# Optimization experiments

Hardware: AMD Instinct MI355X
Metric: run time of the kernel (lower is better)

## Reference

```python
import jax, jax.numpy as jnp
import numpy as np

N = 100000      # nodes
IN_DIM = 128    # input feature dim
HID = 64        # hidden_dim / out_dim per head
HEADS = 4
E_RAND = 1600000  # random edges; self-loops appended -> E = E_RAND + N
SCALES = 3


def setup_inputs() -> dict:
    key = jax.random.key(0)
    ks = jax.random.split(key, 12)
    h = jax.random.normal(ks[0], (N, IN_DIM), dtype=jnp.float32)
    src = jax.random.randint(ks[1], (E_RAND,), 0, N)
    dst = jax.random.randint(ks[2], (E_RAND,), 0, N)
    loop = jnp.arange(N)
    src = jnp.concatenate([src, loop])  # self-loops ensure every dst has a mailbox
    dst = jnp.concatenate([dst, loop])
    frac_cover_mat = jax.random.randint(ks[3], (N, SCALES), 0, N)
    # learned params (bias=False everywhere); xavier-ish scaling
    layer1_fc = jax.random.normal(ks[4], (HEADS, HID, IN_DIM), jnp.float32) / np.sqrt(IN_DIM)
    layer1_attn = jax.random.normal(ks[5], (HEADS, 2 * HID), jnp.float32) * 0.1
    layer2_fc = jax.random.normal(ks[6], (HID, HID * HEADS), jnp.float32) / np.sqrt(HID * HEADS)
    layer2_attn = jax.random.normal(ks[7], (2 * HID,), jnp.float32) * 0.1
    frac_w = jax.random.normal(ks[8], (SCALES, HID, IN_DIM), jnp.float32) / np.sqrt(IN_DIM)
    frac_final_w = jax.random.normal(ks[9], (HID, SCALES * HID), jnp.float32) / np.sqrt(SCALES * HID)
    fc2_w = jax.random.normal(ks[10], (HID, 2 * HID), jnp.float32) / np.sqrt(2 * HID)
    return {"h": h, "src": src, "dst": dst, "frac_cover_mat": frac_cover_mat,
            "layer1_fc": layer1_fc, "layer1_attn": layer1_attn,
            "layer2_fc": layer2_fc, "layer2_attn": layer2_attn,
            "frac_w": frac_w, "frac_final_w": frac_final_w, "fc2_w": fc2_w}


def _gat_layer(z, src, dst, attn_w, n):
    # attn(cat([z_src, z_dst])) == z_src @ a_src + z_dst @ a_dst  (bias-free Linear)
    d = z.shape[1]
    e = jax.nn.leaky_relu(z[src] @ attn_w[:d] + z[dst] @ attn_w[d:])  # [E]
    # segment softmax over incoming edges of each dst node
    m = jax.ops.segment_max(e, dst, num_segments=n)
    ex = jnp.exp(e - m[dst])
    denom = jax.ops.segment_sum(ex, dst, num_segments=n)
    alpha = ex / denom[dst]                                   # [E]
    return jax.ops.segment_sum(alpha[:, None] * z[src], dst, num_segments=n)  # [N, d]


def reference(h, src, dst, frac_cover_mat,
              layer1_fc, layer1_attn, layer2_fc, layer2_attn,
              frac_w, frac_final_w, fc2_w):
    n = h.shape[0]
    # layer1: multi-head GAT, merge='cat'
    heads = []
    for i in range(layer1_fc.shape[0]):
        z = h @ layer1_fc[i].T                                # [N, HID]
        heads.append(_gat_layer(z, src, dst, layer1_attn[i], n))
    h_nei = jax.nn.elu(jnp.concatenate(heads, axis=1))        # [N, HID*HEADS]
    # layer2: single-head GAT
    z2 = h_nei @ layer2_fc.T                                  # [N, HID]
    h_nei = _gat_layer(z2, src, dst, layer2_attn, n)          # [N, HID]
    # fractal layer (dropout = identity in eval)
    h_all = [h[frac_cover_mat[:, s]] @ frac_w[s].T for s in range(frac_w.shape[0])]
    h_frac = jnp.concatenate(h_all, axis=1) @ frac_final_w.T  # [N, HID]
    # fc2 on cat([h_nei, h_frac]); dropout identity
    h_global = jnp.concatenate([h_nei, h_frac], axis=1) @ fc2_w.T  # [N, HID]
    # AvgPooling over single graph -> [1, HID]
    return jnp.mean(h_global, axis=0, keepdims=True)
```

## Files before the change

kernel.cpp:

```cpp
#include <hip/hip_runtime.h>
#include <math.h>


#define CAP 128

typedef unsigned int  uint_t;
typedef unsigned short ushort_t;
typedef __attribute__((ext_vector_type(8))) short short8;
typedef __attribute__((ext_vector_type(4))) float floatx4;
typedef __attribute__((ext_vector_type(2))) float floatx2;

__device__ __forceinline__ float wred_sum(float v){
#pragma unroll
  for (int o = 1; o < 64; o <<= 1) v += __shfl_xor(v, o, 64);
  return v;
}
__device__ __forceinline__ float lrelu(float x){ return x >= 0.f ? x : 0.01f*x; }
__device__ __forceinline__ ushort_t f2b(float f){
  uint_t u = __float_as_uint(f);
  u = (u + 0x7FFFu + ((u >> 16) & 1u)) >> 16;
  return (ushort_t)u;
}
__device__ __forceinline__ float b2f_lo(uint_t w){ return __uint_as_float(w << 16); }
__device__ __forceinline__ float b2f_hi(uint_t w){ return __uint_as_float(w & 0xFFFF0000u); }

__global__ void k_wpack(const float* __restrict__ W1, const float* __restrict__ W2,
                        const float* __restrict__ a1, const float* __restrict__ a2,
                        ushort_t* __restrict__ w1bp, float* __restrict__ v2){
  __shared__ float v[8][128];
  const int bx = blockIdx.x, t = threadIdx.x;
  if (bx < 128){
    int idx = bx*256 + t;
    int j = idx & 7, lane = (idx >> 3) & 63, ks = (idx >> 9) & 3, tt = idx >> 11;
    int n = tt*16 + (lane & 15), k = ks*32 + (lane >> 4)*8 + j;
    w1bp[idx] = f2b(W1[n*128 + k]);
  } else if (bx == 128){
    for (int o = t; o < 1024; o += 256){
      int col = o >> 7, k = o & 127, hh = col & 3, off = (col >> 2)*64;
      float s = 0.f;
      for (int n = 0; n < 64; n++) s += a1[hh*128 + off + n] * W1[(hh*64 + n)*128 + k];
      v[col][k] = s;
    }
    __syncthreads();
    for (int idx = t; idx < 2048; idx += 256){
      int j = idx & 7, lane = (idx >> 3) & 63, ks = idx >> 9;
      int col = lane & 15, k = ks*32 + (lane >> 4)*8 + j;
      w1bp[32768 + idx] = (col < 8) ? f2b(v[col][k]) : (ushort_t)0;
    }
  } else {
    float s0 = 0.f, s1 = 0.f;
    for (int j = 0; j < 64; j++){
      float wjk = W2[j*256 + t];
      s0 += wjk * a2[j];
      s1 += wjk * a2[64 + j];
    }
    v2[t] = s0; v2[256 + t] = s1;
  }
}

__global__ __launch_bounds__(512) void k_gemm1m(const float* __restrict__ h,
    const ushort_t* __restrict__ w1bp,
    uint_t* __restrict__ z8, float* __restrict__ s1s, float* __restrict__ s1d, int N)
{
  __shared__ __align__(16) ushort_t ldsB[34816];
  const int tid = threadIdx.x;
  {
    const uint4* src = (const uint4*)w1bp;
    uint4* dst = (uint4*)ldsB;
    for (int i = tid; i < 4352; i += 512) dst[i] = src[i];
  }
  __syncthreads();
  const int wave = tid >> 6, lane = tid & 63;
  const int quad = lane >> 4, l16 = lane & 15;
  const int row0 = blockIdx.x*128 + wave*16;
  if (row0 >= N) return;
  const int ar = (row0 + l16 < N) ? (row0 + l16) : (N - 1);
  floatx4 c[17];
#pragma unroll
  for (int t = 0; t < 17; t++) c[t] = (floatx4){0.f,0.f,0.f,0.f};
#pragma unroll
  for (int ks = 0; ks < 4; ks++){
    const float* ap = &h[(size_t)ar*128 + ks*32 + quad*8];
    float4 v0 = *(const float4*)ap;
    float4 v1 = *(const float4*)(ap + 4);
    float vv[8] = {v0.x,v0.y,v0.z,v0.w,v1.x,v1.y,v1.z,v1.w};
    short8 ahi, alo;
#pragma unroll
    for (int j = 0; j < 8; j++){
      ushort_t hb = f2b(vv[j]);
      float hf = __uint_as_float((uint_t)hb << 16);
      ahi[j] = (short)hb;
      alo[j] = (short)f2b(vv[j] - hf);
    }
#pragma unroll
    for (int t = 0; t < 17; t++){
      short8 b = *(const short8*)&ldsB[(size_t)((t*4 + ks)*64 + lane)*8];
      c[t] = __builtin_amdgcn_mfma_f32_16x16x32_bf16(ahi, b, c[t], 0, 0, 0);
    }
    {
      short8 b = *(const short8*)&ldsB[(size_t)((16*4 + ks)*64 + lane)*8];
      c[16] = __builtin_amdgcn_mfma_f32_16x16x32_bf16(alo, b, c[16], 0, 0, 0);
    }
  }
#pragma unroll
  for (int i = 0; i < 4; i++){
    const int r = row0 + quad*4 + i;
    if (r >= N) continue;
#pragma unroll
    for (int m = 0; m < 4; m++){
      int u = 0;
      u = __builtin_amdgcn_cvt_pk_fp8_f32(c[0*4+m][i], c[1*4+m][i], u, false);
      u = __builtin_amdgcn_cvt_pk_fp8_f32(c[2*4+m][i], c[3*4+m][i], u, true);
      z8[(size_t)r*64 + m*16 + l16] = (uint_t)u;
    }
    const float sv = c[16][i];
    if (l16 < 4) s1s[r*4 + l16] = sv;
    else if (l16 < 8) s1d[r*4 + (l16 - 4)] = sv;
  }
}

__global__ void k_hist(const int* __restrict__ d, int* __restrict__ deg, int E){
  int i = blockIdx.x*256 + threadIdx.x;
  if (i < E) atomicAdd(&deg[d[i]], 1);
}
__global__ __launch_bounds__(256) void k_scan1(const int* __restrict__ deg, int* __restrict__ part){
  __shared__ int tmp[256];
  int t = threadIdx.x;
  tmp[t] = deg[blockIdx.x*256 + t];
  __syncthreads();
  for (int off = 128; off > 0; off >>= 1){
    if (t < off) tmp[t] += tmp[t+off];
    __syncthreads();
  }
  if (t == 0) part[blockIdx.x] = tmp[0];
}
__global__ __launch_bounds__(512) void k_scan2(int* __restrict__ part, int B){
  __shared__ int tmp[512];
  int t = threadIdx.x;
  int v = (t < B) ? part[t] : 0;
  tmp[t] = v; __syncthreads();
  for (int off = 1; off < 512; off <<= 1){
    int x = (t >= off) ? tmp[t-off] : 0;
    __syncthreads();
    tmp[t] += x;
    __syncthreads();
  }
  if (t < B) part[t] = tmp[t] - v;
}
__global__ __launch_bounds__(256) void k_scan3(const int* __restrict__ deg, const int* __restrict__ part,
    int* __restrict__ rowptr, int* __restrict__ cursor){
  __shared__ int tmp[256];
  int t = threadIdx.x, i = blockIdx.x*256 + t;
  int v = deg[i];
  tmp[t] = v; __syncthreads();
  for (int off = 1; off < 256; off <<= 1){
    int x = (t >= off) ? tmp[t-off] : 0;
    __syncthreads();
    tmp[t] += x;
    __syncthreads();
  }
  int excl = tmp[t] - v + part[blockIdx.x];
  rowptr[i] = excl; cursor[i] = excl;
}
__global__ void k_scatter(const int* __restrict__ s, const int* __restrict__ d,
    int* __restrict__ cursor, int* __restrict__ csr, int E){
  int i = blockIdx.x*256 + threadIdx.x;
  if (i < E){
    int p = atomicAdd(&cursor[d[i]], 1);
    csr[p] = s[i];
  }
}

__global__ __launch_bounds__(256) void k_gat1(
    const uint_t* __restrict__ z8, const float* __restrict__ s1src, const float* __restrict__ s1dst,
    const int* __restrict__ rowptr, const int* __restrict__ csr, const float* __restrict__ v2,
    uint_t* __restrict__ hneib, float* __restrict__ s2s, float* __restrict__ s2d, int N)
{
  __shared__ int   sbuf[4][CAP];
  __shared__ __align__(16) float4 ebuf[4][CAP];
  __shared__ float v2s[512];
  const int tid = threadIdx.x;
  v2s[tid] = v2[tid];
  v2s[tid + 256] = v2[tid + 256];
  __syncthreads();
  const int wave = tid >> 6, lane = tid & 63;
  const int dst = blockIdx.x*4 + wave;
  if (dst >= N) return;
  const int beg = rowptr[dst];
  const int deg = rowptr[dst+1] - beg;
  const float4 sd = *(const float4*)&s1dst[dst*4];
  float t0=0.f,t1=0.f,t2=0.f,t3=0.f;
  for (int j = lane; j < deg; j += 64){
    int s = csr[beg+j];
    float4 sv = *(const float4*)&s1src[s*4];
    float4 a;
    a.x = __expf(lrelu(sv.x+sd.x)); a.y = __expf(lrelu(sv.y+sd.y));
    a.z = __expf(lrelu(sv.z+sd.z)); a.w = __expf(lrelu(sv.w+sd.w));
    if (j < CAP){ sbuf[wave][j] = s; ebuf[wave][j] = a; }
    t0 += a.x; t1 += a.y; t2 += a.z; t3 += a.w;
  }
  const float inv[4] = {1.f/wred_sum(t0), 1.f/wred_sum(t1), 1.f/wred_sum(t2), 1.f/wred_sum(t3)};
  const int eh = lane >> 5, li = lane & 31;
  float acc[2][4] = {};
  int jj = 0;
  if (deg <= CAP){
    for (; jj + 2 <= deg; jj += 2){
      const int j = jj + eh;
      int s = sbuf[wave][j]; float4 al = ebuf[wave][j];
      uint2 u = *((const uint2*)(z8 + (size_t)s*64) + li);
      floatx2 p0 = __builtin_amdgcn_cvt_pk_f32_fp8(u.x, false);
      floatx2 p1 = __builtin_amdgcn_cvt_pk_f32_fp8(u.x, true);
      floatx2 p2 = __builtin_amdgcn_cvt_pk_f32_fp8(u.y, false);
      floatx2 p3 = __builtin_amdgcn_cvt_pk_f32_fp8(u.y, true);
      acc[0][0] += al.x * p0.x;
      acc[0][1] += al.y * p0.y;
      acc[0][2] += al.z * p1.x;
      acc[0][3] += al.w * p1.y;
      acc[1][0] += al.x * p2.x;
      acc[1][1] += al.y * p2.y;
      acc[1][2] += al.z * p3.x;
      acc[1][3] += al.w * p3.y;
    }
    if (jj < deg && eh == 0){
      int s = sbuf[wave][jj]; float4 al = ebuf[wave][jj];
      uint2 u = *((const uint2*)(z8 + (size_t)s*64) + li);
      floatx2 p0 = __builtin_amdgcn_cvt_pk_f32_fp8(u.x, false);
      floatx2 p1 = __builtin_amdgcn_cvt_pk_f32_fp8(u.x, true);
      floatx2 p2 = __builtin_amdgcn_cvt_pk_f32_fp8(u.y, false);
      floatx2 p3 = __builtin_amdgcn_cvt_pk_f32_fp8(u.y, true);
      acc[0][0] += al.x * p0.x;
      acc[0][1] += al.y * p0.y;
      acc[0][2] += al.z * p1.x;
      acc[0][3] += al.w * p1.y;
      acc[1][0] += al.x * p2.x;
      acc[1][1] += al.y * p2.y;
      acc[1][2] += al.z * p3.x;
      acc[1][3] += al.w * p3.y;
    }
  } else {
    for (; jj < deg; jj += 2){
      const int j = jj + eh;
      const bool v = j < deg;
      const int jc = v ? j : jj;
      int s; float4 al;
      if (jc < CAP){ s = sbuf[wave][jc]; al = ebuf[wave][jc]; }
      else {
        s = csr[beg+jc];
        float4 sv = *(const float4*)&s1src[s*4];
        al.x = __expf(lrelu(sv.x+sd.x)); al.y = __expf(lrelu(sv.y+sd.y));
        al.z = __expf(lrelu(sv.z+sd.z)); al.w = __expf(lrelu(sv.w+sd.w));
      }
      if (!v){ al.x=0.f; al.y=0.f; al.z=0.f; al.w=0.f; }
      uint2 u = *((const uint2*)(z8 + (size_t)s*64) + li);
      floatx2 p0 = __builtin_amdgcn_cvt_pk_f32_fp8(u.x, false);
      floatx2 p1 = __builtin_amdgcn_cvt_pk_f32_fp8(u.x, true);
      floatx2 p2 = __builtin_amdgcn_cvt_pk_f32_fp8(u.y, false);
      floatx2 p3 = __builtin_amdgcn_cvt_pk_f32_fp8(u.y, true);
      acc[0][0] += al.x * p0.x;
      acc[0][1] += al.y * p0.y;
      acc[0][2] += al.z * p1.x;
      acc[0][3] += al.w * p1.y;
      acc[1][0] += al.x * p2.x;
      acc[1][1] += al.y * p2.y;
      acc[1][2] += al.z * p3.x;
      acc[1][3] += al.w * p3.y;
    }
  }
#pragma unroll
  for (int k = 0; k < 2; k++)
#pragma unroll
    for (int hh = 0; hh < 4; hh++) acc[k][hh] += __shfl_xor(acc[k][hh], 32, 64);
  const float* vv = &v2s[eh*256];
  float p = 0.f;
#pragma unroll
  for (int hh = 0; hh < 4; hh++){
    float e0 = acc[0][hh]*inv[hh]; e0 = e0 > 0.f ? e0 : expm1f(e0);
    float e1 = acc[1][hh]*inv[hh]; e1 = e1 > 0.f ? e1 : expm1f(e1);
    p += e0 * vv[hh*64 + 2*li] + e1 * vv[hh*64 + 2*li + 1];
    if (eh == 0)
      hneib[(size_t)dst*128 + hh*32 + li] = (uint_t)f2b(e0) | ((uint_t)f2b(e1) << 16);
  }
#pragma unroll
  for (int o = 1; o < 32; o <<= 1) p += __shfl_xor(p, o, 64);
  if (lane == 0)  s2s[dst] = p;
  if (lane == 32) s2d[dst] = p;
}

__global__ __launch_bounds__(256) void k_aw2(
    const float* __restrict__ s2s, const float* __restrict__ s2d,
    const int* __restrict__ rowptr, const int* __restrict__ csr,
    float* __restrict__ wsrc, int N)
{
  __shared__ int   sbuf[4][CAP];
  __shared__ float ebuf[4][CAP];
  const int wave = threadIdx.x >> 6, lane = threadIdx.x & 63;
  const int dst = blockIdx.x*4 + wave;
  if (dst >= N) return;
  const int beg = rowptr[dst], deg = rowptr[dst+1] - beg;
  const float sd = s2d[dst];
  float ts = 0.f;
  for (int j = lane; j < deg; j += 64){
    int s = csr[beg+j];
    float a = __expf(lrelu(s2s[s] + sd));
    if (j < CAP){ sbuf[wave][j] = s; ebuf[wave][j] = a; }
    ts += a;
  }
  const float inv = 1.f/wred_sum(ts);
  for (int j = lane; j < deg; j += 64){
    int s; float a;
    if (j < CAP){ s = sbuf[wave][j]; a = ebuf[wave][j]; }
    else { s = csr[beg+j]; a = __expf(lrelu(s2s[s] + sd)); }
    atomicAdd(&wsrc[s], a * inv);
  }
}

__global__ __launch_bounds__(256) void k_hsum(const uint_t* __restrict__ hneib,
    const float* __restrict__ wsrc, float* __restrict__ acc256, int N)
{
  __shared__ float pr[512];
  const int t = threadIdx.x;
  const int h2 = t >> 7, p = t & 127;
  float a0 = 0.f, a1 = 0.f;
  const int step = gridDim.x * 2;
  for (int n = blockIdx.x*2 + h2; n < N; n += step){
    float wn = wsrc[n];
    uint_t u = hneib[(size_t)n*128 + p];
    a0 += wn * b2f_lo(u);
    a1 += wn * b2f_hi(u);
  }
  pr[h2*256 + 2*p]     = a0;
  pr[h2*256 + 2*p + 1] = a1;
  __syncthreads();
  float v = pr[t] + pr[256 + t];
  int pp = t >> 1;
  int d = (pp >> 5)*64 + 2*(pp & 31) + (t & 1);
  atomicAdd(&acc256[d], v);
}

__global__ __launch_bounds__(256) void k_frac(const float* __restrict__ h,
    const int* __restrict__ fcm, float* __restrict__ accFrac, int N)
{
  __shared__ float red[8][384];
  const int tid = threadIdx.x;
  const int wave = tid >> 6, lane = tid & 63;
  const int g = lane >> 5, li = lane & 31;
  const int stream0 = blockIdx.x*8 + wave*2 + g;
  const int step = gridDim.x * 8;
  float4 a0 = {0,0,0,0}, a1 = {0,0,0,0}, a2 = {0,0,0,0};
  for (int n = stream0; n < N; n += step){
    int i0 = fcm[n*3], i1 = fcm[n*3+1], i2 = fcm[n*3+2];
    float4 v0 = *(const float4*)&h[(size_t)i0*128 + li*4];
    float4 v1 = *(const float4*)&h[(size_t)i1*128 + li*4];
    float4 v2 = *(const float4*)&h[(size_t)i2*128 + li*4];
    a0.x += v0.x; a0.y += v0.y; a0.z += v0.z; a0.w += v0.w;
    a1.x += v1.x; a1.y += v1.y; a1.z += v1.z; a1.w += v1.w;
    a2.x += v2.x; a2.y += v2.y; a2.z += v2.z; a2.w += v2.w;
  }
  const int w8 = wave*2 + g;
  *(float4*)&red[w8][0*128 + li*4] = a0;
  *(float4*)&red[w8][1*128 + li*4] = a1;
  *(float4*)&red[w8][2*128 + li*4] = a2;
  __syncthreads();
  for (int i = tid; i < 384; i += 256){
    float v = 0.f;
#pragma unroll
    for (int w = 0; w < 8; w++) v += red[w][i];
    atomicAdd(&accFrac[i], v);
  }
}

__global__ __launch_bounds__(256) void k_finalize(const float* __restrict__ acc256,
    const float* __restrict__ accFrac, const float* __restrict__ W2,
    const float* __restrict__ frw, const float* __restrict__ frf,
    const float* __restrict__ fc2, float* __restrict__ out, float invN)
{
  __shared__ float mh[256], nei[64], g[384], mm[192], hfrac[64];
  int t = threadIdx.x;
  mh[t] = acc256[t] * invN;
  for (int i = t; i < 384; i += 256) g[i] = accFrac[i] * invN;
  __syncthreads();
  if (t < 64){
    float s = 0.f;
    for (int k = 0; k < 256; k++) s += W2[t*256 + k] * mh[k];
    nei[t] = s;
  }
  for (int i = t; i < 192; i += 256){
    int s = i >> 6, d = i & 63;
    const float* w = frw + (size_t)(s*64 + d)*128;
    const float* gs = g + s*128;
    float sum = 0.f;
    for (int k = 0; k < 128; k++) sum += gs[k]*w[k];
    mm[i] = sum;
  }
  __syncthreads();
  if (t < 64){
    float s = 0.f;
    for (int k = 0; k < 192; k++) s += mm[k]*frf[t*192 + k];
    hfrac[t] = s;
  }
  __syncthreads();
  if (t < 64){
    float o = 0.f;
    for (int k = 0; k < 64; k++)
      o += fc2[t*128 + k]*nei[k] + fc2[t*128 + 64 + k]*hfrac[k];
    out[t] = o;
  }
}

extern "C" void kernel_launch(void* const* d_in, const int* in_sizes, int n_in,
                              void* d_out, int out_size, void* d_ws, size_t ws_size,
                              hipStream_t stream)
{
  const float* h    = (const float*)d_in[0];
  const int*   srcI = (const int*)  d_in[1];
  const int*   dstI = (const int*)  d_in[2];
  const int*   fcm  = (const int*)  d_in[3];
  const float* l1fc = (const float*)d_in[4];
  const float* l1at = (const float*)d_in[5];
  const float* l2fc = (const float*)d_in[6];
  const float* l2at = (const float*)d_in[7];
  const float* frw  = (const float*)d_in[8];
  const float* frf  = (const float*)d_in[9];
  const float* fc2  = (const float*)d_in[10];
  float* out = (float*)d_out;
  (void)n_in; (void)out_size; (void)ws_size;

  const int N = in_sizes[0] / 128;
  const int E = in_sizes[1];
  const int B = (N + 256) / 256;
  const int PAD = B * 256;

  char* w = (char*)d_ws;
  size_t off = 0;
  auto alloc = [&](size_t bytes) -> char* {
    char* p = w + off; off = (off + bytes + 255) & ~(size_t)255; return p;
  };
  uint_t* z8    = (uint_t*)alloc((size_t)N*64*4);
  uint_t* hneib = (uint_t*)alloc((size_t)N*128*4);
  float* s1s  = (float*)alloc((size_t)N*4*4);
  float* s1d  = (float*)alloc((size_t)N*4*4);
  float* s2s  = (float*)alloc((size_t)N*4);
  float* s2d  = (float*)alloc((size_t)N*4);
  int*   deg     = (int*)  alloc((size_t)PAD*4);
  float* wsrc    = (float*)alloc((size_t)N*4);
  float* acc256  = (float*)alloc(256*4);
  float* accFrac = (float*)alloc(384*4);
  const size_t zbytes = (size_t)((char*)accFrac + 384*4 - (char*)deg);
  int*   rowptr = (int*)alloc((size_t)PAD*4);
  int*   cursor = (int*)alloc((size_t)PAD*4);
  int*   part   = (int*)alloc(512*4);
  int*   csr    = (int*)alloc((size_t)E*4);
  ushort_t* w1bp = (ushort_t*)alloc(34816*2);
  float* v2     = (float*)alloc(512*4);

  hipMemsetAsync(deg, 0, zbytes, stream);

  hipLaunchKernelGGL(k_wpack,   dim3(130),           dim3(256), 0, stream,
                     l1fc, l2fc, l1at, l2at, w1bp, v2);
  hipLaunchKernelGGL(k_hist,    dim3((E+255)/256),   dim3(256), 0, stream, dstI, deg, E);
  hipLaunchKernelGGL(k_scan1,   dim3(B),             dim3(256), 0, stream, deg, part);
  hipLaunchKernelGGL(k_scan2,   dim3(1),             dim3(512), 0, stream, part, B);
  hipLaunchKernelGGL(k_scan3,   dim3(B),             dim3(256), 0, stream, deg, part, rowptr, cursor);
  hipLaunchKernelGGL(k_scatter, dim3((E+255)/256),   dim3(256), 0, stream, srcI, dstI, cursor, csr, E);
  hipLaunchKernelGGL(k_gemm1m,  dim3((N+127)/128),   dim3(512), 0, stream,
                     h, w1bp, z8, s1s, s1d, N);
  hipLaunchKernelGGL(k_gat1,    dim3((N+3)/4),       dim3(256), 0, stream,
                     z8, s1s, s1d, rowptr, csr, v2, hneib, s2s, s2d, N);
  hipLaunchKernelGGL(k_aw2,     dim3((N+3)/4),       dim3(256), 0, stream,
                     s2s, s2d, rowptr, csr, wsrc, N);
  hipLaunchKernelGGL(k_hsum,    dim3(608),           dim3(256), 0, stream,
                     hneib, wsrc, acc256, N);
  hipLaunchKernelGGL(k_frac,    dim3(1024),          dim3(256), 0, stream, h, fcm, accFrac, N);
  hipLaunchKernelGGL(k_finalize,dim3(1),             dim3(256), 0, stream,
                     acc256, accFrac, l2fc, frw, frf, fc2, out, 1.0f/(float)N);
}
```

Before: 626.5 us.

## Merge independent stages into combined kernels to overlap GEMM, CSR scatter and fractal sums

Weight packing and degree histogram are folded into one prep kernel using extra blocks with a grid-stride loop. The layer-1 GEMM, CSR scatter and fractal gather-sum are merged into a single kernel that dispatches on block index, so these independent stages run concurrently. This cuts launch count and lets the memory-bound scatter and gather overlap with the MFMA GEMM. In exchange, every block now reserves the largest shared-memory footprint (68 KB), which can reduce occupancy for the scatter and frac blocks.

Measured after the change: 614.7 us. Within noise of the previous version (-1.9%).

```diff
diff --git a/kernel.cpp b/kernel.cpp
--- a/kernel.cpp
+++ b/kernel.cpp
@@ -24,9 +24,11 @@
 __device__ __forceinline__ float b2f_lo(uint_t w){ return __uint_as_float(w << 16); }
 __device__ __forceinline__ float b2f_hi(uint_t w){ return __uint_as_float(w & 0xFFFF0000u); }
 
-__global__ void k_wpack(const float* __restrict__ W1, const float* __restrict__ W2,
-                        const float* __restrict__ a1, const float* __restrict__ a2,
-                        ushort_t* __restrict__ w1bp, float* __restrict__ v2){
+__global__ void k_prep(const float* __restrict__ W1, const float* __restrict__ W2,
+                       const float* __restrict__ a1, const float* __restrict__ a2,
+                       const int* __restrict__ dstI, int E,
+                       ushort_t* __restrict__ w1bp, float* __restrict__ v2,
+                       int* __restrict__ deg){
   __shared__ float v[8][128];
   const int bx = blockIdx.x, t = threadIdx.x;
   if (bx < 128){
@@ -47,7 +49,7 @@
       int col = lane & 15, k = ks*32 + (lane >> 4)*8 + j;
       w1bp[32768 + idx] = (col < 8) ? f2b(v[col][k]) : (ushort_t)0;
     }
-  } else {
+  } else if (bx == 129){
     float s0 = 0.f, s1 = 0.f;
     for (int j = 0; j < 64; j++){
       float wjk = W2[j*256 + t];
@@ -55,74 +57,13 @@
       s1 += wjk * a2[64 + j];
     }
     v2[t] = s0; v2[256 + t] = s1;
-  }
-}
-
-__global__ __launch_bounds__(512) void k_gemm1m(const float* __restrict__ h,
-    const ushort_t* __restrict__ w1bp,
-    uint_t* __restrict__ z8, float* __restrict__ s1s, float* __restrict__ s1d, int N)
-{
-  __shared__ __align__(16) ushort_t ldsB[34816];
-  const int tid = threadIdx.x;
-  {
-    const uint4* src = (const uint4*)w1bp;
-    uint4* dst = (uint4*)ldsB;
-    for (int i = tid; i < 4352; i += 512) dst[i] = src[i];
-  }
-  __syncthreads();
-  const int wave = tid >> 6, lane = tid & 63;
-  const int quad = lane >> 4, l16 = lane & 15;
-  const int row0 = blockIdx.x*128 + wave*16;
-  if (row0 >= N) return;
-  const int ar = (row0 + l16 < N) ? (row0 + l16) : (N - 1);
-  floatx4 c[17];
-#pragma unroll
-  for (int t = 0; t < 17; t++) c[t] = (floatx4){0.f,0.f,0.f,0.f};
-#pragma unroll
-  for (int ks = 0; ks < 4; ks++){
-    const float* ap = &h[(size_t)ar*128 + ks*32 + quad*8];
-    float4 v0 = *(const float4*)ap;
-    float4 v1 = *(const float4*)(ap + 4);
-    float vv[8] = {v0.x,v0.y,v0.z,v0.w,v1.x,v1.y,v1.z,v1.w};
-    short8 ahi, alo;
-#pragma unroll
-    for (int j = 0; j < 8; j++){
-      ushort_t hb = f2b(vv[j]);
-      float hf = __uint_as_float((uint_t)hb << 16);
-      ahi[j] = (short)hb;
-      alo[j] = (short)f2b(vv[j] - hf);
-    }
-#pragma unroll
-    for (int t = 0; t < 17; t++){
-      short8 b = *(const short8*)&ldsB[(size_t)((t*4 + ks)*64 + lane)*8];
-      c[t] = __builtin_amdgcn_mfma_f32_16x16x32_bf16(ahi, b, c[t], 0, 0, 0);
-    }
-    {
-      short8 b = *(const short8*)&ldsB[(size_t)((16*4 + ks)*64 + lane)*8];
-      c[16] = __builtin_amdgcn_mfma_f32_16x16x32_bf16(alo, b, c[16], 0, 0, 0);
-    }
-  }
-#pragma unroll
-  for (int i = 0; i < 4; i++){
-    const int r = row0 + quad*4 + i;
-    if (r >= N) continue;
-#pragma unroll
-    for (int m = 0; m < 4; m++){
-      int u = 0;
-      u = __builtin_amdgcn_cvt_pk_fp8_f32(c[0*4+m][i], c[1*4+m][i], u, false);
-      u = __builtin_amdgcn_cvt_pk_fp8_f32(c[2*4+m][i], c[3*4+m][i], u, true);
-      z8[(size_t)r*64 + m*16 + l16] = (uint_t)u;
-    }
-    const float sv = c[16][i];
-    if (l16 < 4) s1s[r*4 + l16] = sv;
-    else if (l16 < 8) s1d[r*4 + (l16 - 4)] = sv;
-  }
-}
-
-__global__ void k_hist(const int* __restrict__ d, int* __restrict__ deg, int E){
-  int i = blockIdx.x*256 + threadIdx.x;
-  if (i < E) atomicAdd(&deg[d[i]], 1);
-}
+  } else {
+    const int nb = gridDim.x - 130;
+    for (int i = (bx-130)*256 + t; i < E; i += nb*256)
+      atomicAdd(&deg[dstI[i]], 1);
+  }
+}
+
 __global__ __launch_bounds__(256) void k_scan1(const int* __restrict__ deg, int* __restrict__ part){
   __shared__ int tmp[256];
   int t = threadIdx.x;
@@ -162,12 +103,105 @@
   int excl = tmp[t] - v + part[blockIdx.x];
   rowptr[i] = excl; cursor[i] = excl;
 }
-__global__ void k_scatter(const int* __restrict__ s, const int* __restrict__ d,
-    int* __restrict__ cursor, int* __restrict__ csr, int E){
-  int i = blockIdx.x*256 + threadIdx.x;
-  if (i < E){
-    int p = atomicAdd(&cursor[d[i]], 1);
-    csr[p] = s[i];
+
+__global__ __launch_bounds__(512) void k_mega(const float* __restrict__ h,
+    const ushort_t* __restrict__ w1bp,
+    uint_t* __restrict__ z8, float* __restrict__ s1s, float* __restrict__ s1d, int N,
+    const int* __restrict__ srcI, const int* __restrict__ dstI,
+    int* __restrict__ cursor, int* __restrict__ csr, int E, int Gg, int Gs,
+    const int* __restrict__ fcm, float* __restrict__ accFrac)
+{
+  static __shared__ __align__(16) char smem[69632];
+  const int bx = blockIdx.x, tid = threadIdx.x;
+  if (bx < Gg){
+    ushort_t* ldsB = (ushort_t*)smem;
+    {
+      const uint4* src = (const uint4*)w1bp;
+      uint4* dst = (uint4*)ldsB;
+      for (int i = tid; i < 4352; i += 512) dst[i] = src[i];
+    }
+    __syncthreads();
+    const int wave = tid >> 6, lane = tid & 63;
+    const int quad = lane >> 4, l16 = lane & 15;
+    const int row0 = bx*128 + wave*16;
+    if (row0 >= N) return;
+    const int ar = (row0 + l16 < N) ? (row0 + l16) : (N - 1);
+    floatx4 c[17];
+#pragma unroll
+    for (int t = 0; t < 17; t++) c[t] = (floatx4){0.f,0.f,0.f,0.f};
+#pragma unroll
+    for (int ks = 0; ks < 4; ks++){
+      const float* ap = &h[(size_t)ar*128 + ks*32 + quad*8];
+      float4 v0 = *(const float4*)ap;
+      float4 v1 = *(const float4*)(ap + 4);
+      float vv[8] = {v0.x,v0.y,v0.z,v0.w,v1.x,v1.y,v1.z,v1.w};
+      short8 ahi, alo;
+#pragma unroll
+      for (int j = 0; j < 8; j++){
+        ushort_t hb = f2b(vv[j]);
+        float hf = __uint_as_float((uint_t)hb << 16);
+        ahi[j] = (short)hb;
+        alo[j] = (short)f2b(vv[j] - hf);
+      }
+#pragma unroll
+      for (int t = 0; t < 17; t++){
+        short8 b = *(const short8*)&ldsB[(size_t)((t*4 + ks)*64 + lane)*8];
+        c[t] = __builtin_amdgcn_mfma_f32_16x16x32_bf16(ahi, b, c[t], 0, 0, 0);
+      }
+      {
+        short8 b = *(const short8*)&ldsB[(size_t)((16*4 + ks)*64 + lane)*8];
+        c[16] = __builtin_amdgcn_mfma_f32_16x16x32_bf16(alo, b, c[16], 0, 0, 0);
+      }
+    }
+#pragma unroll
+    for (int i = 0; i < 4; i++){
+      const int r = row0 + quad*4 + i;
+      if (r >= N) continue;
+#pragma unroll
+      for (int m = 0; m < 4; m++){
+        int u = 0;
+        u = __builtin_amdgcn_cvt_pk_fp8_f32(c[0*4+m][i], c[1*4+m][i], u, false);
+        u = __builtin_amdgcn_cvt_pk_fp8_f32(c[2*4+m][i], c[3*4+m][i], u, true);
+        z8[(size_t)r*64 + m*16 + l16] = (uint_t)u;
+      }
+      const float sv = c[16][i];
+      if (l16 < 4) s1s[r*4 + l16] = sv;
+      else if (l16 < 8) s1d[r*4 + (l16 - 4)] = sv;
+    }
+  } else if (bx < Gg + Gs){
+    const int i = (bx - Gg)*512 + tid;
+    if (i < E){
+      int p = atomicAdd(&cursor[dstI[i]], 1);
+      csr[p] = srcI[i];
+    }
+  } else {
+    float (*red)[384] = (float(*)[384])smem;
+    const int wave = tid >> 6, lane = tid & 63;
+    const int g = lane >> 5, li = lane & 31;
+    const int Gf = gridDim.x - Gg - Gs;
+    const int stream0 = (bx - Gg - Gs)*16 + wave*2 + g;
+    const int step = Gf * 16;
+    float4 a0 = {0,0,0,0}, a1 = {0,0,0,0}, a2 = {0,0,0,0};
+    for (int n = stream0; n < N; n += step){
+      int i0 = fcm[n*3], i1 = fcm[n*3+1], i2 = fcm[n*3+2];
+      float4 v0 = *(const float4*)&h[(size_t)i0*128 + li*4];
+      float4 v1 = *(const float4*)&h[(size_t)i1*128 + li*4];
+      float4 v2 = *(const float4*)&h[(size_t)i2*128 + li*4];
+      a0.x += v0.x; a0.y += v0.y; a0.z += v0.z; a0.w += v0.w;
+      a1.x += v1.x; a1.y += v1.y; a1.z += v1.z; a1.w += v1.w;
+      a2.x += v2.x; a2.y += v2.y; a2.z += v2.z; a2.w += v2.w;
+    }
+    const int w16 = wave*2 + g;
+    *(float4*)&red[w16][0*128 + li*4] = a0;
+    *(float4*)&red[w16][1*128 + li*4] = a1;
+    *(float4*)&red[w16][2*128 + li*4] = a2;
+    __syncthreads();
+    for (int i = tid; i < 384; i += 512){
+      float v = 0.f;
+#pragma unroll
+      for (int w = 0; w < 16; w++) v += red[w][i];
+      atomicAdd(&accFrac[i], v);
+    }
   }
 }
 
@@ -337,38 +371,6 @@
   atomicAdd(&acc256[d], v);
 }
 
-__global__ __launch_bounds__(256) void k_frac(const float* __restrict__ h,
-    const int* __restrict__ fcm, float* __restrict__ accFrac, int N)
-{
-  __shared__ float red[8][384];
-  const int tid = threadIdx.x;
-  const int wave = tid >> 6, lane = tid & 63;
-  const int g = lane >> 5, li = lane & 31;
-  const int stream0 = blockIdx.x*8 + wave*2 + g;
-  const int step = gridDim.x * 8;
-  float4 a0 = {0,0,0,0}, a1 = {0,0,0,0}, a2 = {0,0,0,0};
-  for (int n = stream0; n < N; n += step){
-    int i0 = fcm[n*3], i1 = fcm[n*3+1], i2 = fcm[n*3+2];
-    float4 v0 = *(const float4*)&h[(size_t)i0*128 + li*4];
-    float4 v1 = *(const float4*)&h[(size_t)i1*128 + li*4];
-    float4 v2 = *(const float4*)&h[(size_t)i2*128 + li*4];
-    a0.x += v0.x; a0.y += v0.y; a0.z += v0.z; a0.w += v0.w;
-    a1.x += v1.x; a1.y += v1.y; a1.z += v1.z; a1.w += v1.w;
-    a2.x += v2.x; a2.y += v2.y; a2.z += v2.z; a2.w += v2.w;
-  }
-  const int w8 = wave*2 + g;
-  *(float4*)&red[w8][0*128 + li*4] = a0;
-  *(float4*)&red[w8][1*128 + li*4] = a1;
-  *(float4*)&red[w8][2*128 + li*4] = a2;
-  __syncthreads();
-  for (int i = tid; i < 384; i += 256){
-    float v = 0.f;
-#pragma unroll
-    for (int w = 0; w < 8; w++) v += red[w][i];
-    atomicAdd(&accFrac[i], v);
-  }
-}
-
 __global__ __launch_bounds__(256) void k_finalize(const float* __restrict__ acc256,
     const float* __restrict__ accFrac, const float* __restrict__ W2,
     const float* __restrict__ frw, const float* __restrict__ frf,
@@ -455,22 +457,25 @@
 
   hipMemsetAsync(deg, 0, zbytes, stream);
 
-  hipLaunchKernelGGL(k_wpack,   dim3(130),           dim3(256), 0, stream,
-                     l1fc, l2fc, l1at, l2at, w1bp, v2);
-  hipLaunchKernelGGL(k_hist,    dim3((E+255)/256),   dim3(256), 0, stream, dstI, deg, E);
-  hipLaunchKernelGGL(k_scan1,   dim3(B),             dim3(256), 0, stream, deg, part);
-  hipLaunchKernelGGL(k_scan2,   dim3(1),             dim3(512), 0, stream, part, B);
-  hipLaunchKernelGGL(k_scan3,   dim3(B),             dim3(256), 0, stream, deg, part, rowptr, cursor);
-  hipLaunchKernelGGL(k_scatter, dim3((E+255)/256),   dim3(256), 0, stream, srcI, dstI, cursor, csr, E);
-  hipLaunchKernelGGL(k_gemm1m,  dim3((N+127)/128),   dim3(512), 0, stream,
-                     h, w1bp, z8, s1s, s1d, N);
-  hipLaunchKernelGGL(k_gat1,    dim3((N+3)/4),       dim3(256), 0, stream,
+  hipLaunchKernelGGL(k_prep,  dim3(130 + 512), dim3(256), 0, stream,
+                     l1fc, l2fc, l1at, l2at, dstI, E, w1bp, v2, deg);
+  hipLaunchKernelGGL(k_scan1, dim3(B),   dim3(256), 0, stream, deg, part);
+  hipLaunchKernelGGL(k_scan2, dim3(1),   dim3(512), 0, stream, part, B);
+  hipLaunchKernelGGL(k_scan3, dim3(B),   dim3(256), 0, stream, deg, part, rowptr, cursor);
+
+  const int Gg = (N + 127) / 128;
+  const int Gs = (E + 511) / 512;
+  const int Gf = 512;
+  hipLaunchKernelGGL(k_mega,  dim3(Gg + Gs + Gf), dim3(512), 0, stream,
+                     h, w1bp, z8, s1s, s1d, N,
+                     srcI, dstI, cursor, csr, E, Gg, Gs,
+                     fcm, accFrac);
+  hipLaunchKernelGGL(k_gat1,  dim3((N+3)/4), dim3(256), 0, stream,
                      z8, s1s, s1d, rowptr, csr, v2, hneib, s2s, s2d, N);
-  hipLaunchKernelGGL(k_aw2,     dim3((N+3)/4),       dim3(256), 0, stream,
+  hipLaunchKernelGGL(k_aw2,   dim3((N+3)/4), dim3(256), 0, stream,
                      s2s, s2d, rowptr, csr, wsrc, N);
-  hipLaunchKernelGGL(k_hsum,    dim3(608),           dim3(256), 0, stream,
+  hipLaunchKernelGGL(k_hsum,  dim3(608),     dim3(256), 0, stream,
                      hneib, wsrc, acc256, N);
-  hipLaunchKernelGGL(k_frac,    dim3(1024),          dim3(256), 0, stream, h, fcm, accFrac, N);
-  hipLaunchKernelGGL(k_finalize,dim3(1),             dim3(256), 0, stream,
+  hipLaunchKernelGGL(k_finalize, dim3(1),    dim3(256), 0, stream,
                      acc256, accFrac, l2fc, frw, frf, fc2, out, 1.0f/(float)N);
 }
```
